# Optimization experiments

Hardware: AMD Instinct MI355X
Metric: run time of the kernel (lower is better)

The kernel has to match this reference:

```python
import jax, jax.numpy as jnp
import numpy as np

S, L, IN_DIM, PROJ, OUT = 128, 512, 256, 32, 128


def _layernorm(x, eps=1e-5):
    mu = jnp.mean(x, axis=-1, keepdims=True)
    var = jnp.var(x, axis=-1, keepdims=True)
    return (x - mu) * jax.lax.rsqrt(var + eps)


def setup_inputs() -> dict:
    key = jax.random.key(0)
    k0, k1, k2 = jax.random.split(key, 3)
    return {
        "node_repr": jax.random.normal(k0, (S, L, IN_DIM), dtype=jnp.float32),
        "mask": jnp.ones((S, L), dtype=jnp.float32),
        # nn.Linear(in_dim, 2*proj_dim): weight [2*proj, in], bias [2*proj]
        "w_proj": jax.random.normal(k1, (2 * PROJ, IN_DIM), dtype=jnp.float32) * 0.02,
        "b_proj": jnp.zeros((2 * PROJ,), dtype=jnp.float32),
        "out_weights": jax.random.normal(k2, (PROJ, PROJ, OUT), dtype=jnp.float32) * 0.02,
        "out_bias": jnp.zeros((OUT,), dtype=jnp.float32),
    }


def reference(node_repr, mask, w_proj, b_proj, out_weights, out_bias):
    # normalize over channel dim (parameter-free layer norm, as utils.tnormalize)
    x = _layernorm(node_repr)                     # [s, i, in_dim]
    act = x @ w_proj.T + b_proj                   # [s, i, 2*proj]
    act = act * mask[..., None]
    l = act[..., :PROJ]                           # [s, i, d]
    r = act[..., PROJ:]                           # [s, j, e]
    # norm = einsum('sid,sjd->ijd', mask[...,None], mask[...,None]) -> [i, j, 1]
    norm = jnp.einsum('si,sj->ij', mask, mask)[..., None]
    # outer-product-mean: contract MSA dim s, then mix (d,e) -> f
    out = jnp.einsum('sid,def,sje->ijf', l, out_weights, r, optimize=True)
    out = out + out_bias
    return out / (norm + 0.001)
```

## Files before the change

### kernel.cpp

```cpp
#include <hip/hip_runtime.h>
#include <cstdint>

#define S_DIM 128
#define L_DIM 512
#define INimD 256
#define OUTF  128

typedef __bf16 bf16x8 __attribute__((ext_vector_type(8)));
typedef __bf16 bf16x4 __attribute__((ext_vector_type(4)));
typedef float  f32x16 __attribute__((ext_vector_type(16)));

__device__ __forceinline__ unsigned short f2bf(float f) {
  unsigned int u = __float_as_uint(f);
  u = (u + 0x7fffu + ((u >> 16) & 1u)) >> 16;
  return (unsigned short)u;
}

__device__ __forceinline__ void gload_lds16(const void* gsrc, void* ldst) {
  __builtin_amdgcn_global_load_lds(
      (const __attribute__((address_space(1))) unsigned int*)gsrc,
      (__attribute__((address_space(3))) unsigned int*)ldst, 16, 0, 0);
}

__global__ __launch_bounds__(256) void k_wp(const float* __restrict__ w,
                                            unsigned short* __restrict__ WP)
{
  const int gid = blockIdx.x * 256 + threadIdx.x;
  const int ln = gid & 63, t = gid >> 6;
  const int nt = t & 1, kt = t >> 1;
  const int j  = nt * 32 + (ln & 31);
  const int k0 = kt * 16 + (ln >> 5) * 8;
#pragma unroll
  for (int jj = 0; jj < 8; ++jj)
    WP[(size_t)gid * 8 + jj] = f2bf(w[(size_t)j * INimD + k0 + jj]);
}

__global__ __launch_bounds__(256) void k_lnproj(
    const float* __restrict__ x, const float* __restrict__ mask,
    const unsigned short* __restrict__ WP, const float* __restrict__ b,
    unsigned short* __restrict__ l_t, unsigned short* __restrict__ r_t)
{
  __shared__ unsigned short smem[128 * 256];
  __shared__ float msk[128];
  const int tid = threadIdx.x;
  const int wv = tid >> 6, lane = tid & 63;
  const int half = lane >> 5, ln = lane & 31;
  const int l = blockIdx.x;

  if (tid < 128) msk[tid] = mask[(size_t)tid * L_DIM + l];

  for (int bi = 0; bi < 8; ++bi) {
    const int r0 = wv * 32 + bi * 4;
    float4 v[4];
#pragma unroll
    for (int q = 0; q < 4; ++q)
      v[q] = ((const float4*)(x + ((size_t)(r0 + q) * L_DIM + l) * INimD))[lane];
#pragma unroll
    for (int q = 0; q < 4; ++q) {
      float sm = v[q].x + v[q].y + v[q].z + v[q].w;
      float sq = v[q].x*v[q].x + v[q].y*v[q].y + v[q].z*v[q].z + v[q].w*v[q].w;
#pragma unroll
      for (int off = 32; off > 0; off >>= 1) {
        sm += __shfl_xor(sm, off);
        sq += __shfl_xor(sq, off);
      }
      const float mu  = sm * (1.0f / 256.0f);
      const float var = sq * (1.0f / 256.0f) - mu * mu;
      const float rs  = rsqrtf(var + 1e-5f);
      const int r = r0 + q;
      ushort4 hp;
      hp.x = f2bf((v[q].x - mu) * rs);
      hp.y = f2bf((v[q].y - mu) * rs);
      hp.z = f2bf((v[q].z - mu) * rs);
      hp.w = f2bf((v[q].w - mu) * rs);
      const int col = (lane * 4) ^ ((r & 7) << 3);
      *(ushort4*)&smem[r * 256 + col] = hp;
    }
  }
  __syncthreads();

  f32x16 acc0, acc1;
#pragma unroll
  for (int q = 0; q < 16; ++q) { acc0[q] = 0.f; acc1[q] = 0.f; }
  const int ar = wv * 32 + ln;
#pragma unroll
  for (int kt = 0; kt < 16; ++kt) {
    const int col = (kt * 16 + half * 8) ^ ((ln & 7) << 3);
    bf16x8 a  = *(const bf16x8*)&smem[ar * 256 + col];
    bf16x8 b0 = *(const bf16x8*)(WP + ((size_t)((kt * 2 + 0) * 64 + lane)) * 8);
    bf16x8 b1 = *(const bf16x8*)(WP + ((size_t)((kt * 2 + 1) * 64 + lane)) * 8);
    acc0 = __builtin_amdgcn_mfma_f32_32x32x16_bf16(a, b0, acc0, 0, 0, 0);
    acc1 = __builtin_amdgcn_mfma_f32_32x32x16_bf16(a, b1, acc1, 0, 0, 0);
  }
  __syncthreads();

  unsigned short (*act)[136] = (unsigned short(*)[136])smem;
  const float bj0 = b[ln];
  const float bj1 = b[32 + ln];
#pragma unroll
  for (int nt = 0; nt < 2; ++nt) {
    const f32x16 a = nt ? acc1 : acc0;
    const float bj = nt ? bj1 : bj0;
    const int j = nt * 32 + ln;
#pragma unroll
    for (int g = 0; g < 4; ++g) {
      const int s0 = wv * 32 + g * 8 + half * 4;
      ushort4 p;
      p.x = f2bf((a[g*4+0] + bj) * msk[s0+0]);
      p.y = f2bf((a[g*4+1] + bj) * msk[s0+1]);
      p.z = f2bf((a[g*4+2] + bj) * msk[s0+2]);
      p.w = f2bf((a[g*4+3] + bj) * msk[s0+3]);
      *(ushort4*)&act[j][s0] = p;
    }
  }
  __syncthreads();

  const int d = tid >> 2, c = (tid & 3) * 32;
  uint4 outv[4];
  ushort4* pv = (ushort4*)outv;
#pragma unroll
  for (int q = 0; q < 8; ++q) pv[q] = *(ushort4*)&act[d][c + q * 4];
  unsigned short* dst = (d < 32)
      ? (l_t + ((size_t)l * 32 + d) * S_DIM + c)
      : (r_t + ((size_t)l * 32 + (d - 32)) * S_DIM + c);
  ((uint4*)dst)[0] = outv[0];
  ((uint4*)dst)[1] = outv[1];
  ((uint4*)dst)[2] = outv[2];
  ((uint4*)dst)[3] = outv[3];
}

__global__ __launch_bounds__(256) void k_norm(const float* __restrict__ mask,
                                              float* __restrict__ recip)
{
  __shared__ float mi[128][16];
  __shared__ float mj[128][16];
  const int i0 = blockIdx.y * 16, j0 = blockIdx.x * 16;
  for (int idx = threadIdx.x; idx < 2048; idx += 256) {
    const int s = idx >> 4, cc = idx & 15;
    mi[s][cc] = mask[(size_t)s * L_DIM + i0 + cc];
    mj[s][cc] = mask[(size_t)s * L_DIM + j0 + cc];
  }
  __syncthreads();
  const int ti = threadIdx.x >> 4, tj = threadIdx.x & 15;
  float acc = 0.f;
#pragma unroll 8
  for (int s = 0; s < 128; ++s) acc += mi[s][ti] * mj[s][tj];
  recip[(size_t)(i0 + ti) * L_DIM + j0 + tj] = 1.0f / (acc + 0.001f);
}

__global__ __launch_bounds__(256) void k_wb(const float* __restrict__ W,
                                            unsigned short* __restrict__ WB)
{
  const int gid = blockIdx.x * 256 + threadIdx.x;
  const int ln = gid & 63;
  const int ftkt = gid >> 6;
  const int ft = ftkt & 3, kt = ftkt >> 2;
  const int f  = ft * 32 + (ln & 31);
  const int kb = kt * 16 + (ln >> 5) * 8;
#pragma unroll
  for (int jj = 0; jj < 8; ++jj) {
    const int k = kb + jj;
    WB[(size_t)gid * 8 + jj] = f2bf(W[(size_t)k * OUTF + f]);
  }
}

__global__ __launch_bounds__(256, 3) void k_pair(
    const unsigned short* __restrict__ l_t, const unsigned short* __restrict__ r_t,
    const unsigned short* __restrict__ WB, const float* __restrict__ recip,
    const float* __restrict__ bias, float* __restrict__ out)
{
  __shared__ __align__(16) unsigned short l_lds[2][32][128];
  __shared__ __align__(16) unsigned short g_lds[2][64][68];
  const int tid = threadIdx.x;
  const int wv = tid >> 6, lane = tid & 63;
  const int half = lane >> 5, ln = lane & 31;
  const int j0 = blockIdx.x * 4, i0 = blockIdx.y * 16;

  bf16x8 rf[8];
#pragma unroll
  for (int s8 = 0; s8 < 8; ++s8)
    rf[s8] = *(const bf16x8*)(r_t + ((size_t)(j0 + wv) * 32 + ln) * S_DIM
                                  + s8 * 16 + half * 8);

  const unsigned short* lsrc[2];
#pragma unroll
  for (int t = 0; t < 2; ++t) {
    const int r_ = wv * 8 + t * 4 + (lane >> 4);
    const int gg = lane & 15;
    lsrc[t] = l_t + ((size_t)(i0 + (r_ & 15)) * 32 + (r_ >> 4)) * S_DIM
                  + ((gg ^ (r_ & 7)) * 8);
  }
#pragma unroll
  for (int t = 0; t < 2; ++t)
    gload_lds16(lsrc[t], &l_lds[0][wv * 8 + t * 4][0]);

  f32x16 acc0, acc1;
#pragma unroll
  for (int q = 0; q < 16; ++q) { acc0[q] = 0.f; acc1[q] = 0.f; }

  const int pr  = (ln & 15) * 4 + wv;
  const int dcc = ln >> 4;

  __syncthreads();

  for (int c = 0; c < 16; ++c) {
    const int cur = c & 1;
    if (c < 15) {
#pragma unroll
      for (int t = 0; t < 2; ++t) {
        lsrc[t] += 256;
        gload_lds16(lsrc[t], &l_lds[cur ^ 1][wv * 8 + t * 4][0]);
      }
    }
    bf16x8 bw[4];
#pragma unroll
    for (int kt = 0; kt < 4; ++kt)
      bw[kt] = *(const bf16x8*)(WB + ((size_t)((c * 4 + kt) * 4 + wv) * 64 + lane) * 8);

    f32x16 g;
#pragma unroll
    for (int q = 0; q < 16; ++q) g[q] = 0.f;
#pragma unroll
    for (int s8 = 0; s8 < 8; ++s8) {
      const int col = ((s8 * 2 + half) ^ (ln & 7)) * 8;
      bf16x8 bl = *(const bf16x8*)&l_lds[cur][ln][col];
      g = __builtin_amdgcn_mfma_f32_32x32x16_bf16(rf[s8], bl, g, 0, 0, 0);
    }
    {
      unsigned short* gp = &g_lds[cur][pr][dcc * 32 + 4 * half];
#pragma unroll
      for (int q = 0; q < 4; ++q) {
        ushort4 hp;
        hp.x = f2bf(g[4*q+0]); hp.y = f2bf(g[4*q+1]);
        hp.z = f2bf(g[4*q+2]); hp.w = f2bf(g[4*q+3]);
        *(ushort4*)(gp + q * 8) = hp;
      }
    }
    __syncthreads();

#pragma unroll
    for (int kt = 0; kt < 4; ++kt) {
      const unsigned short* p0 = &g_lds[cur][ln][kt * 16 + half * 8];
      const unsigned short* p1 = &g_lds[cur][32 + ln][kt * 16 + half * 8];
      bf16x4 a0l = *(const bf16x4*)p0, a0h = *(const bf16x4*)(p0 + 4);
      bf16x4 a1l = *(const bf16x4*)p1, a1h = *(const bf16x4*)(p1 + 4);
      bf16x8 a0 = __builtin_shufflevector(a0l, a0h, 0,1,2,3,4,5,6,7);
      bf16x8 a1 = __builtin_shufflevector(a1l, a1h, 0,1,2,3,4,5,6,7);
      acc0 = __builtin_amdgcn_mfma_f32_32x32x16_bf16(a0, bw[kt], acc0, 0, 0, 0);
      acc1 = __builtin_amdgcn_mfma_f32_32x32x16_bf16(a1, bw[kt], acc1, 0, 0, 0);
    }
  }

  const float bi = bias[wv * 32 + ln];
#pragma unroll
  for (int mt = 0; mt < 2; ++mt) {
    const f32x16 a = mt ? acc1 : acc0;
#pragma unroll
    for (int reg = 0; reg < 16; ++reg) {
      const int p = mt * 32 + (reg & 3) + 8 * (reg >> 2) + 4 * half;
      const int i = i0 + (p >> 2), j = j0 + (p & 3);
      const float val = (a[reg] + bi) * recip[(size_t)i * L_DIM + j];
      out[((size_t)i * L_DIM + j) * OUTF + wv * 32 + ln] = val;
    }
  }
}

extern "C" void kernel_launch(void* const* d_in, const int* in_sizes, int n_in,
                              void* d_out, int out_size, void* d_ws, size_t ws_size,
                              hipStream_t stream) {
  const float* x    = (const float*)d_in[0];
  const float* mask = (const float*)d_in[1];
  const float* w    = (const float*)d_in[2];
  const float* b    = (const float*)d_in[3];
  const float* W    = (const float*)d_in[4];
  const float* bias = (const float*)d_in[5];
  float* out = (float*)d_out;

  char* ws = (char*)d_ws;
  unsigned short* l_t = (unsigned short*)ws;
  unsigned short* r_t = (unsigned short*)(ws + (4u << 20));
  unsigned short* WB  = (unsigned short*)(ws + (8u << 20));
  float* recip = (float*)(ws + (8u << 20) + (512u << 10));
  unsigned short* WP  = (unsigned short*)(ws + (8u << 20) + (512u << 10) + (1u << 20));

  hipLaunchKernelGGL(k_wp,     dim3(8),        dim3(256), 0, stream, w, WP);
  hipLaunchKernelGGL(k_lnproj, dim3(512),      dim3(256), 0, stream, x, mask, WP, b, l_t, r_t);
  hipLaunchKernelGGL(k_norm,   dim3(32, 32),   dim3(256), 0, stream, mask, recip);
  hipLaunchKernelGGL(k_wb,     dim3(64),       dim3(256), 0, stream, W, WB);
  hipLaunchKernelGGL(k_pair,   dim3(128, 32),  dim3(256), 0, stream, l_t, r_t, WB, recip, bias, out);
}
```

Before: 337.4 us.

## Merge prep kernels, prefetch LN rows, reswizzle LDS and raise pair occupancy

Folds the three small prep kernels (mask norm reciprocal, WB and WP bf16 packing) into one launch to cut launch overhead. The layernorm-projection kernel now software-prefetches the next four input rows while the current ones are normalized. The pair kernel drops the padded g_lds layout in favour of an XOR swizzle, widens the l_lds swizzle to 16 keys, remaps the rows of the intermediate product, adds s_setprio around the MFMA sections, and raises the launch-bounds occupancy target from 3 to 4. Together these aim to remove LDS bank conflicts and hide latency, at the risk of register pressure or spills under the tighter occupancy bound.

```diff
diff --git a/kernel.cpp b/kernel.cpp
--- a/kernel.cpp
+++ b/kernel.cpp
@@ -22,17 +22,49 @@
       (__attribute__((address_space(3))) unsigned int*)ldst, 16, 0, 0);
 }
 
-__global__ __launch_bounds__(256) void k_wp(const float* __restrict__ w,
-                                            unsigned short* __restrict__ WP)
+__global__ __launch_bounds__(256) void k_prep(
+    const float* __restrict__ mask, float* __restrict__ recip,
+    const float* __restrict__ W, unsigned short* __restrict__ WB,
+    const float* __restrict__ w, unsigned short* __restrict__ WP)
 {
-  const int gid = blockIdx.x * 256 + threadIdx.x;
-  const int ln = gid & 63, t = gid >> 6;
-  const int nt = t & 1, kt = t >> 1;
-  const int j  = nt * 32 + (ln & 31);
-  const int k0 = kt * 16 + (ln >> 5) * 8;
-#pragma unroll
-  for (int jj = 0; jj < 8; ++jj)
-    WP[(size_t)gid * 8 + jj] = f2bf(w[(size_t)j * INimD + k0 + jj]);
+  __shared__ float mi[128][16];
+  __shared__ float mj[128][16];
+  const int t = blockIdx.x;
+  if (t < 1024) {
+    const int i0 = (t >> 5) * 16, j0 = (t & 31) * 16;
+    for (int idx = threadIdx.x; idx < 2048; idx += 256) {
+      const int s = idx >> 4, cc = idx & 15;
+      mi[s][cc] = mask[(size_t)s * L_DIM + i0 + cc];
+      mj[s][cc] = mask[(size_t)s * L_DIM + j0 + cc];
+    }
+    __syncthreads();
+    const int ti = threadIdx.x >> 4, tj = threadIdx.x & 15;
+    float acc = 0.f;
+#pragma unroll 8
+    for (int s = 0; s < 128; ++s) acc += mi[s][ti] * mj[s][tj];
+    recip[(size_t)(i0 + ti) * L_DIM + j0 + tj] = 1.0f / (acc + 0.001f);
+  } else if (t < 1088) {
+    const int gid = (t - 1024) * 256 + threadIdx.x;
+    const int ln = gid & 63;
+    const int ftkt = gid >> 6;
+    const int ft = ftkt & 3, kt = ftkt >> 2;
+    const int f  = ft * 32 + (ln & 31);
+    const int kb = kt * 16 + (ln >> 5) * 8;
+#pragma unroll
+    for (int jj = 0; jj < 8; ++jj) {
+      const int k = kb + jj;
+      WB[(size_t)gid * 8 + jj] = f2bf(W[(size_t)k * OUTF + f]);
+    }
+  } else {
+    const int gid = (t - 1088) * 256 + threadIdx.x;
+    const int ln = gid & 63, tt = gid >> 6;
+    const int nt = tt & 1, kt = tt >> 1;
+    const int j  = nt * 32 + (ln & 31);
+    const int k0 = kt * 16 + (ln >> 5) * 8;
+#pragma unroll
+    for (int jj = 0; jj < 8; ++jj)
+      WP[(size_t)gid * 8 + jj] = f2bf(w[(size_t)j * INimD + k0 + jj]);
+  }
 }
 
 __global__ __launch_bounds__(256) void k_lnproj(
@@ -49,12 +81,18 @@
 
   if (tid < 128) msk[tid] = mask[(size_t)tid * L_DIM + l];
 
+  float4 v[4];
+#pragma unroll
+  for (int q = 0; q < 4; ++q)
+    v[q] = ((const float4*)(x + ((size_t)(wv * 32 + q) * L_DIM + l) * INimD))[lane];
   for (int bi = 0; bi < 8; ++bi) {
     const int r0 = wv * 32 + bi * 4;
-    float4 v[4];
-#pragma unroll
-    for (int q = 0; q < 4; ++q)
-      v[q] = ((const float4*)(x + ((size_t)(r0 + q) * L_DIM + l) * INimD))[lane];
+    float4 vn[4];
+    if (bi < 7) {
+#pragma unroll
+      for (int q = 0; q < 4; ++q)
+        vn[q] = ((const float4*)(x + ((size_t)(r0 + 4 + q) * L_DIM + l) * INimD))[lane];
+    }
 #pragma unroll
     for (int q = 0; q < 4; ++q) {
       float sm = v[q].x + v[q].y + v[q].z + v[q].w;
@@ -76,6 +114,8 @@
       const int col = (lane * 4) ^ ((r & 7) << 3);
       *(ushort4*)&smem[r * 256 + col] = hp;
     }
+#pragma unroll
+    for (int q = 0; q < 4; ++q) v[q] = vn[q];
   }
   __syncthreads();
 
@@ -129,48 +169,13 @@
   ((uint4*)dst)[3] = outv[3];
 }
 
-__global__ __launch_bounds__(256) void k_norm(const float* __restrict__ mask,
-                                              float* __restrict__ recip)
-{
-  __shared__ float mi[128][16];
-  __shared__ float mj[128][16];
-  const int i0 = blockIdx.y * 16, j0 = blockIdx.x * 16;
-  for (int idx = threadIdx.x; idx < 2048; idx += 256) {
-    const int s = idx >> 4, cc = idx & 15;
-    mi[s][cc] = mask[(size_t)s * L_DIM + i0 + cc];
-    mj[s][cc] = mask[(size_t)s * L_DIM + j0 + cc];
-  }
-  __syncthreads();
-  const int ti = threadIdx.x >> 4, tj = threadIdx.x & 15;
-  float acc = 0.f;
-#pragma unroll 8
-  for (int s = 0; s < 128; ++s) acc += mi[s][ti] * mj[s][tj];
-  recip[(size_t)(i0 + ti) * L_DIM + j0 + tj] = 1.0f / (acc + 0.001f);
-}
-
-__global__ __launch_bounds__(256) void k_wb(const float* __restrict__ W,
-                                            unsigned short* __restrict__ WB)
-{
-  const int gid = blockIdx.x * 256 + threadIdx.x;
-  const int ln = gid & 63;
-  const int ftkt = gid >> 6;
-  const int ft = ftkt & 3, kt = ftkt >> 2;
-  const int f  = ft * 32 + (ln & 31);
-  const int kb = kt * 16 + (ln >> 5) * 8;
-#pragma unroll
-  for (int jj = 0; jj < 8; ++jj) {
-    const int k = kb + jj;
-    WB[(size_t)gid * 8 + jj] = f2bf(W[(size_t)k * OUTF + f]);
-  }
-}
-
-__global__ __launch_bounds__(256, 3) void k_pair(
+__global__ __launch_bounds__(256, 4) void k_pair(
     const unsigned short* __restrict__ l_t, const unsigned short* __restrict__ r_t,
     const unsigned short* __restrict__ WB, const float* __restrict__ recip,
     const float* __restrict__ bias, float* __restrict__ out)
 {
   __shared__ __align__(16) unsigned short l_lds[2][32][128];
-  __shared__ __align__(16) unsigned short g_lds[2][64][68];
+  __shared__ __align__(16) unsigned short g_lds[2][64][64];
   const int tid = threadIdx.x;
   const int wv = tid >> 6, lane = tid & 63;
   const int half = lane >> 5, ln = lane & 31;
@@ -188,7 +193,7 @@
     const int r_ = wv * 8 + t * 4 + (lane >> 4);
     const int gg = lane & 15;
     lsrc[t] = l_t + ((size_t)(i0 + (r_ & 15)) * 32 + (r_ >> 4)) * S_DIM
-                  + ((gg ^ (r_ & 7)) * 8);
+                  + ((gg ^ (r_ & 15)) * 8);
   }
 #pragma unroll
   for (int t = 0; t < 2; ++t)
@@ -198,8 +203,8 @@
 #pragma unroll
   for (int q = 0; q < 16; ++q) { acc0[q] = 0.f; acc1[q] = 0.f; }
 
-  const int pr  = (ln & 15) * 4 + wv;
-  const int dcc = ln >> 4;
+  const int prow = wv * 16 + (ln & 15);
+  const int dcc  = ln >> 4;
 
   __syncthreads();
 
@@ -220,35 +225,46 @@
     f32x16 g;
 #pragma unroll
     for (int q = 0; q < 16; ++q) g[q] = 0.f;
+    __builtin_amdgcn_s_setprio(1);
 #pragma unroll
     for (int s8 = 0; s8 < 8; ++s8) {
-      const int col = ((s8 * 2 + half) ^ (ln & 7)) * 8;
+      const int col = (((s8 * 2 + half) ^ (ln & 15))) * 8;
       bf16x8 bl = *(const bf16x8*)&l_lds[cur][ln][col];
       g = __builtin_amdgcn_mfma_f32_32x32x16_bf16(rf[s8], bl, g, 0, 0, 0);
     }
+    __builtin_amdgcn_s_setprio(0);
     {
-      unsigned short* gp = &g_lds[cur][pr][dcc * 32 + 4 * half];
+      unsigned short* g0 = &g_lds[cur][prow][0];
+      const int key = prow & 15;
 #pragma unroll
       for (int q = 0; q < 4; ++q) {
         ushort4 hp;
         hp.x = f2bf(g[4*q+0]); hp.y = f2bf(g[4*q+1]);
         hp.z = f2bf(g[4*q+2]); hp.w = f2bf(g[4*q+3]);
-        *(ushort4*)(gp + q * 8) = hp;
+        const int u8 = (8 * dcc + 2 * q + half) ^ key;
+        *(ushort4*)(g0 + u8 * 4) = hp;
       }
     }
     __syncthreads();
 
+    __builtin_amdgcn_s_setprio(1);
 #pragma unroll
     for (int kt = 0; kt < 4; ++kt) {
-      const unsigned short* p0 = &g_lds[cur][ln][kt * 16 + half * 8];
-      const unsigned short* p1 = &g_lds[cur][32 + ln][kt * 16 + half * 8];
-      bf16x4 a0l = *(const bf16x4*)p0, a0h = *(const bf16x4*)(p0 + 4);
-      bf16x4 a1l = *(const bf16x4*)p1, a1h = *(const bf16x4*)(p1 + 4);
+      const int b8 = kt * 4 + 2 * half;
+      const int r0_ = ln,     k0 = r0_ & 15;
+      const int r1_ = 32 + ln, k1 = r1_ & 15;
+      const unsigned short* gp0 = &g_lds[cur][r0_][0];
+      const unsigned short* gp1 = &g_lds[cur][r1_][0];
+      bf16x4 a0l = *(const bf16x4*)(gp0 + ((b8    ) ^ k0) * 4);
+      bf16x4 a0h = *(const bf16x4*)(gp0 + ((b8 + 1) ^ k0) * 4);
+      bf16x4 a1l = *(const bf16x4*)(gp1 + ((b8    ) ^ k1) * 4);
+      bf16x4 a1h = *(const bf16x4*)(gp1 + ((b8 + 1) ^ k1) * 4);
       bf16x8 a0 = __builtin_shufflevector(a0l, a0h, 0,1,2,3,4,5,6,7);
       bf16x8 a1 = __builtin_shufflevector(a1l, a1h, 0,1,2,3,4,5,6,7);
       acc0 = __builtin_amdgcn_mfma_f32_32x32x16_bf16(a0, bw[kt], acc0, 0, 0, 0);
       acc1 = __builtin_amdgcn_mfma_f32_32x32x16_bf16(a1, bw[kt], acc1, 0, 0, 0);
     }
+    __builtin_amdgcn_s_setprio(0);
   }
 
   const float bi = bias[wv * 32 + ln];
@@ -257,7 +273,8 @@
     const f32x16 a = mt ? acc1 : acc0;
 #pragma unroll
     for (int reg = 0; reg < 16; ++reg) {
-      const int p = mt * 32 + (reg & 3) + 8 * (reg >> 2) + 4 * half;
+      const int rr = (reg & 3) + 8 * (reg >> 2) + 4 * half;
+      const int p  = (rr & 15) * 4 + mt * 2 + (rr >> 4);
       const int i = i0 + (p >> 2), j = j0 + (p & 3);
       const float val = (a[reg] + bi) * recip[(size_t)i * L_DIM + j];
       out[((size_t)i * L_DIM + j) * OUTF + wv * 32 + ln] = val;
@@ -283,9 +300,7 @@
   float* recip = (float*)(ws + (8u << 20) + (512u << 10));
   unsigned short* WP  = (unsigned short*)(ws + (8u << 20) + (512u << 10) + (1u << 20));
 
-  hipLaunchKernelGGL(k_wp,     dim3(8),        dim3(256), 0, stream, w, WP);
+  hipLaunchKernelGGL(k_prep,   dim3(1096),     dim3(256), 0, stream, mask, recip, W, WB, w, WP);
   hipLaunchKernelGGL(k_lnproj, dim3(512),      dim3(256), 0, stream, x, mask, WP, b, l_t, r_t);
-  hipLaunchKernelGGL(k_norm,   dim3(32, 32),   dim3(256), 0, stream, mask, recip);
-  hipLaunchKernelGGL(k_wb,     dim3(64),       dim3(256), 0, stream, W, WB);
   hipLaunchKernelGGL(k_pair,   dim3(128, 32),  dim3(256), 0, stream, l_t, r_t, WB, recip, bias, out);
 }
```

New measurement: 385.6 us. 1.14x slower.
